# Optimization experiments

Hardware: AMD Instinct MI355X
Metric: run time of the kernel (lower is better)

Reference implementation:

```python
import jax, jax.numpy as jnp
import numpy as np

SORB = 64      # spin orbitals (sequence length)
NELE = 32      # electrons
H = 512        # num_hiddens
B = 4096       # batch
ALPHA = NELE // 2                      # = beta = 16 (spin-up / spin-down electrons)
MIN_I = min(SORB - 2 * ALPHA, 2 * ALPHA)  # = 32; symmetry mask active for i >= MIN_I
EPS = 1e-12


def setup_inputs() -> dict:
    key = jax.random.key(0)
    ks = jax.random.split(key, 10)
    s_in = 1.0 / np.sqrt(2.0)
    s_h = 1.0 / np.sqrt(H)
    return {
        "x": jax.random.randint(ks[0], (B, SORB), 0, 2, dtype=jnp.int32),  # occupancies {0,1}
        "W_ih0": jax.random.normal(ks[1], (3 * H, 2), jnp.float32) * s_in,   # GRU layer0 input weights (r,z,n)
        "W_hh0": jax.random.normal(ks[2], (3 * H, H), jnp.float32) * s_h,
        "W_ih1": jax.random.normal(ks[3], (3 * H, H), jnp.float32) * s_h,    # GRU layer1
        "W_hh1": jax.random.normal(ks[4], (3 * H, H), jnp.float32) * s_h,
        "W_amp": jax.random.normal(ks[5], (2, H), jnp.float32) * s_h,
        "b_amp": jax.random.normal(ks[6], (2,), jnp.float32) * 0.01,
        "W_phase": jax.random.normal(ks[7], (2, H), jnp.float32) * s_h,
        "b_phase": jax.random.normal(ks[8], (2,), jnp.float32) * 0.01,
    }


def _gru_cell(x_in, h, Wih, Whh):
    # PyTorch GRU (bias=False), gate order r, z, n
    gi = x_in @ Wih.T          # (B, 3H)
    gh = h @ Whh.T             # (B, 3H)
    r = jax.nn.sigmoid(gi[:, :H] + gh[:, :H])
    z = jax.nn.sigmoid(gi[:, H:2 * H] + gh[:, H:2 * H])
    n = jnp.tanh(gi[:, 2 * H:] + r * gh[:, 2 * H:])
    return (1.0 - z) * n + z * h


def reference(x, W_ih0, W_hh0, W_ih1, W_hh1, W_amp, b_amp, W_phase, b_phase):
    dt = W_ih0.dtype
    bits = x.astype(jnp.int32)           # (B, SORB) occupancies
    nb = bits.shape[0]

    def step(carry, inp):
        h0, h1, x0, amp, phase, nup, ndn = carry
        i, b_i = inp                      # site index, occupancy bits (B,)
        h0n = _gru_cell(x0, h0, W_ih0, W_hh0)
        h1n = _gru_cell(h0n, h1, W_ih1, W_hh1)
        y = h1n                           # (B, H)
        # amplitude: sqrt(softmax(linear))
        y_amp = jnp.sqrt(jax.nn.softmax(y @ W_amp.T + b_amp, axis=1))   # (B, 2)
        # phase: pi * softsign(linear)
        ph = y @ W_phase.T + b_phase
        y_ph = jnp.pi * ph / (1.0 + jnp.abs(ph))
        # particle-number symmetry mask (alpha == beta spin sectors)
        is_even = (i % 2) == 0            # even sites: spin-up, odd: spin-down
        cnt = jnp.where(is_even, nup, ndn)
        lower = (ALPHA - SORB // 2 + i // 2).astype(dt)
        occ_ok = (cnt < ALPHA).astype(dt)
        unocc_ok = (cnt > lower).astype(dt)
        mask = jnp.stack([unocc_ok, occ_ok], axis=1)
        masked = y_amp * mask
        masked = masked / jnp.sqrt(jnp.sum(masked * masked, axis=1, keepdims=True) + EPS)
        y_amp = jnp.where(i >= MIN_I, masked, y_amp)
        # accumulate conditional amplitude / phase at the sampled occupancy
        sel_a = jnp.take_along_axis(y_amp, b_i[:, None], axis=1)[:, 0]
        sel_p = jnp.take_along_axis(y_ph, b_i[:, None], axis=1)[:, 0]
        amp = amp * sel_a
        phase = phase + sel_p
        bf = b_i.astype(dt)
        nup = nup + jnp.where(is_even, bf, 0.0)
        ndn = ndn + jnp.where(is_even, 0.0, bf)
        x0n = jax.nn.one_hot(b_i, 2, dtype=dt)  # next-step GRU input
        return (h0n, h1n, x0n, amp, phase, nup, ndn), None

    init = (
        jnp.zeros((nb, H), dt), jnp.zeros((nb, H), dt), jnp.zeros((nb, 2), dt),
        jnp.ones((nb,), dt), jnp.zeros((nb,), dt), jnp.zeros((nb,), dt), jnp.zeros((nb,), dt),
    )
    xs = (jnp.arange(SORB), bits.T)       # scan over sites
    (_, _, _, amp, phase, _, _), _ = jax.lax.scan(step, init, xs)
    # complex wavefunction psi = amp * exp(1j*phase); returned as real pair (amp, phase)
    return jnp.stack([amp, phase], axis=-1)
```

## Files before the change

kernel.cpp:

```cpp
#include <hip/hip_runtime.h>
#include <hip/hip_bf16.h>

#define SORB  64
#define HID   512
#define BATCH 4096
#define N3H   1536
#define KD    512
#define BK    64
#define PI_F  3.14159265358979f

typedef _Float16 half8 __attribute__((ext_vector_type(8)));
typedef float    floatx4 __attribute__((ext_vector_type(4)));

__device__ __forceinline__ void gload16(const void* g, void* l) {
    __builtin_amdgcn_global_load_lds(
        (const __attribute__((address_space(1))) void*)g,
        (__attribute__((address_space(3))) void*)l, 16, 0, 0);
}

__device__ __forceinline__ float sigmoidf_(float x) { return 1.f / (1.f + __expf(-x)); }
__device__ __forceinline__ float tanhf_(float x) {
    x = fminf(fmaxf(x, -15.f), 15.f);
    const float e2 = __expf(2.f * x);
    return (e2 - 1.f) / (e2 + 1.f);
}

__global__ __launch_bounds__(256) void convw_kernel(
    const float* __restrict__ w0, const float* __restrict__ w1, const float* __restrict__ w2,
    _Float16* __restrict__ o0, _Float16* __restrict__ o1, _Float16* __restrict__ o2)
{
    const int i = blockIdx.x * 256 + threadIdx.x;
    if (i < N3H * KD) {
        o0[i] = (_Float16)w0[i];
        o1[i] = (_Float16)w1[i];
        o2[i] = (_Float16)w2[i];
    }
}

__global__ __launch_bounds__(256) void init_kernel(
    float* __restrict__ amp, float* __restrict__ phase,
    int* __restrict__ nup, int* __restrict__ ndn)
{
    const int i = blockIdx.x * 256 + threadIdx.x;
    if (i < BATCH) { amp[i] = 1.f; phase[i] = 0.f; nup[i] = 0; ndn[i] = 0; }
}


__global__ __launch_bounds__(256) void step1_kernel(
    const _Float16* __restrict__ h0h_c, const _Float16* __restrict__ h1h_c,
    const _Float16* __restrict__ wh0,   const _Float16* __restrict__ wh1,
    const float* __restrict__ Wih0, const int* __restrict__ bits,
    float* __restrict__ h0f, _Float16* __restrict__ h0h_n,
    _Float16* __restrict__ gB, int step)
{
    const int z = blockIdx.z;
    const _Float16* A = z ? h1h_c : h0h_c;
    const _Float16* W = z ? wh1 : wh0;
    const int j0 = blockIdx.x * 64;
    const int m0 = blockIdx.y * 64;

    __shared__ __align__(16) _Float16 As[64 * BK];
    __shared__ __align__(16) _Float16 Bs[192 * BK];

    const int tid  = threadIdx.x;
    const int lane = tid & 63;
    const int wid  = tid >> 6;
    const int wm   = wid >> 1, wj = wid & 1;

    floatx4 acc[2][2][3];
    const floatx4 z4 = {0.f, 0.f, 0.f, 0.f};
#pragma unroll
    for (int a = 0; a < 2; ++a)
#pragma unroll
        for (int b = 0; b < 2; ++b)
#pragma unroll
            for (int g = 0; g < 3; ++g) acc[a][b][g] = z4;

    const _Float16* a_srcp[2];
#pragma unroll
    for (int k2 = 0; k2 < 2; ++k2) {
        const int p = tid + k2 * 256, row = p >> 3, c = (p & 7) ^ (row & 7);
        a_srcp[k2] = A + (size_t)(m0 + row) * KD + c * 8;
    }
    const _Float16* b_srcp[6];
#pragma unroll
    for (int k2 = 0; k2 < 6; ++k2) {
        const int p = tid + k2 * 256, row = p >> 3, c = (p & 7) ^ (row & 7);
        const int grow = (row >> 6) * HID + j0 + (row & 63);
        b_srcp[k2] = W + (size_t)grow * KD + c * 8;
    }
    _Float16* a_dst[2];
#pragma unroll
    for (int k2 = 0; k2 < 2; ++k2) a_dst[k2] = As + (size_t)(k2 * 256 + wid * 64) * 8;
    _Float16* b_dst[6];
#pragma unroll
    for (int k2 = 0; k2 < 6; ++k2) b_dst[k2] = Bs + (size_t)(k2 * 256 + wid * 64) * 8;

    const int ku = lane >> 4;
    int aoff[2][2], boff[2][3][2];
#pragma unroll
    for (int mf = 0; mf < 2; ++mf) {
        const int r = wm * 32 + mf * 16 + (lane & 15);
#pragma unroll
        for (int kk = 0; kk < 2; ++kk)
            aoff[mf][kk] = r * BK + (((kk * 4 + ku) ^ (r & 7)) * 8);
    }
#pragma unroll
    for (int jf = 0; jf < 2; ++jf)
#pragma unroll
        for (int g = 0; g < 3; ++g) {
            const int r = g * 64 + wj * 32 + jf * 16 + (lane & 15);
#pragma unroll
            for (int kk = 0; kk < 2; ++kk)
                boff[jf][g][kk] = r * BK + (((kk * 4 + ku) ^ (r & 7)) * 8);
        }

    for (int kt = 0; kt < 8; ++kt) {
        const int k0 = kt * BK;
#pragma unroll
        for (int k2 = 0; k2 < 2; ++k2) gload16(a_srcp[k2] + k0, a_dst[k2]);
#pragma unroll
        for (int k2 = 0; k2 < 6; ++k2) gload16(b_srcp[k2] + k0, b_dst[k2]);
        __syncthreads();
#pragma unroll
        for (int kk = 0; kk < 2; ++kk) {
            half8 af[2], bf[2][3];
#pragma unroll
            for (int mf = 0; mf < 2; ++mf) af[mf] = *(const half8*)(As + aoff[mf][kk]);
#pragma unroll
            for (int jf = 0; jf < 2; ++jf)
#pragma unroll
                for (int g = 0; g < 3; ++g) bf[jf][g] = *(const half8*)(Bs + boff[jf][g][kk]);
#pragma unroll
            for (int mf = 0; mf < 2; ++mf)
#pragma unroll
                for (int jf = 0; jf < 2; ++jf)
#pragma unroll
                    for (int g = 0; g < 3; ++g)
                        acc[mf][jf][g] = __builtin_amdgcn_mfma_f32_16x16x32_f16(af[mf], bf[jf][g], acc[mf][jf][g], 0, 0, 0);
        }
        __syncthreads();
    }

    if (z == 0) {
#pragma unroll
        for (int mf = 0; mf < 2; ++mf)
#pragma unroll
            for (int jf = 0; jf < 2; ++jf) {
                const floatx4 gr = acc[mf][jf][0];
                const floatx4 gz = acc[mf][jf][1];
                const floatx4 gn = acc[mf][jf][2];
#pragma unroll
                for (int reg = 0; reg < 4; ++reg) {
                    const int m = m0 + wm * 32 + mf * 16 + (lane >> 4) * 4 + reg;
                    const int j = j0 + wj * 32 + jf * 16 + (lane & 15);
                    float gir = 0.f, giz = 0.f, gin = 0.f;
                    if (step > 0) {
                        const int t = bits[m * SORB + step - 1];
                        gir = Wih0[j * 2 + t];
                        giz = Wih0[(HID + j) * 2 + t];
                        gin = Wih0[(2 * HID + j) * 2 + t];
                    }
                    const float r  = sigmoidf_(gir + gr[reg]);
                    const float zz = sigmoidf_(giz + gz[reg]);
                    const float n  = tanhf_(gin + r * gn[reg]);
                    const size_t idx = (size_t)m * HID + j;
                    const float h  = h0f[idx];
                    const float hn = (1.f - zz) * n + zz * h;
                    h0f[idx]   = hn;
                    h0h_n[idx] = (_Float16)hn;
                }
            }
    } else {
#pragma unroll
        for (int mf = 0; mf < 2; ++mf)
#pragma unroll
            for (int jf = 0; jf < 2; ++jf)
#pragma unroll
                for (int g = 0; g < 3; ++g)
#pragma unroll
                    for (int reg = 0; reg < 4; ++reg) {
                        const int m = m0 + wm * 32 + mf * 16 + (lane >> 4) * 4 + reg;
                        const int j = j0 + wj * 32 + jf * 16 + (lane & 15);
                        gB[(size_t)m * N3H + g * HID + j] = (_Float16)acc[mf][jf][g][reg];
                    }
    }
}

__global__ __launch_bounds__(256) void step2_kernel(
    const _Float16* __restrict__ h0h_n, const _Float16* __restrict__ wi1,
    const _Float16* __restrict__ gB,
    float* __restrict__ h1f, _Float16* __restrict__ h1h_n)
{
    const int j0 = blockIdx.x * 64;
    const int m0 = blockIdx.y * 64;

    __shared__ __align__(16) _Float16 As[64 * BK];
    __shared__ __align__(16) _Float16 Bs[192 * BK];

    const int tid  = threadIdx.x;
    const int lane = tid & 63;
    const int wid  = tid >> 6;
    const int wm   = wid >> 1, wj = wid & 1;

    floatx4 acc[2][2][3];
    const floatx4 z4 = {0.f, 0.f, 0.f, 0.f};
#pragma unroll
    for (int a = 0; a < 2; ++a)
#pragma unroll
        for (int b = 0; b < 2; ++b)
#pragma unroll
            for (int g = 0; g < 3; ++g) acc[a][b][g] = z4;

    const _Float16* a_srcp[2];
#pragma unroll
    for (int k2 = 0; k2 < 2; ++k2) {
        const int p = tid + k2 * 256, row = p >> 3, c = (p & 7) ^ (row & 7);
        a_srcp[k2] = h0h_n + (size_t)(m0 + row) * KD + c * 8;
    }
    const _Float16* b_srcp[6];
#pragma unroll
    for (int k2 = 0; k2 < 6; ++k2) {
        const int p = tid + k2 * 256, row = p >> 3, c = (p & 7) ^ (row & 7);
        const int grow = (row >> 6) * HID + j0 + (row & 63);
        b_srcp[k2] = wi1 + (size_t)grow * KD + c * 8;
    }
    _Float16* a_dst[2];
#pragma unroll
    for (int k2 = 0; k2 < 2; ++k2) a_dst[k2] = As + (size_t)(k2 * 256 + wid * 64) * 8;
    _Float16* b_dst[6];
#pragma unroll
    for (int k2 = 0; k2 < 6; ++k2) b_dst[k2] = Bs + (size_t)(k2 * 256 + wid * 64) * 8;

    const int ku = lane >> 4;
    int aoff[2][2], boff[2][3][2];
#pragma unroll
    for (int mf = 0; mf < 2; ++mf) {
        const int r = wm * 32 + mf * 16 + (lane & 15);
#pragma unroll
        for (int kk = 0; kk < 2; ++kk)
            aoff[mf][kk] = r * BK + (((kk * 4 + ku) ^ (r & 7)) * 8);
    }
#pragma unroll
    for (int jf = 0; jf < 2; ++jf)
#pragma unroll
        for (int g = 0; g < 3; ++g) {
            const int r = g * 64 + wj * 32 + jf * 16 + (lane & 15);
#pragma unroll
            for (int kk = 0; kk < 2; ++kk)
                boff[jf][g][kk] = r * BK + (((kk * 4 + ku) ^ (r & 7)) * 8);
        }

    for (int kt = 0; kt < 8; ++kt) {
        const int k0 = kt * BK;
#pragma unroll
        for (int k2 = 0; k2 < 2; ++k2) gload16(a_srcp[k2] + k0, a_dst[k2]);
#pragma unroll
        for (int k2 = 0; k2 < 6; ++k2) gload16(b_srcp[k2] + k0, b_dst[k2]);
        __syncthreads();
#pragma unroll
        for (int kk = 0; kk < 2; ++kk) {
            half8 af[2], bf[2][3];
#pragma unroll
            for (int mf = 0; mf < 2; ++mf) af[mf] = *(const half8*)(As + aoff[mf][kk]);
#pragma unroll
            for (int jf = 0; jf < 2; ++jf)
#pragma unroll
                for (int g = 0; g < 3; ++g) bf[jf][g] = *(const half8*)(Bs + boff[jf][g][kk]);
#pragma unroll
            for (int mf = 0; mf < 2; ++mf)
#pragma unroll
                for (int jf = 0; jf < 2; ++jf)
#pragma unroll
                    for (int g = 0; g < 3; ++g)
                        acc[mf][jf][g] = __builtin_amdgcn_mfma_f32_16x16x32_f16(af[mf], bf[jf][g], acc[mf][jf][g], 0, 0, 0);
        }
        __syncthreads();
    }

#pragma unroll
    for (int mf = 0; mf < 2; ++mf)
#pragma unroll
        for (int jf = 0; jf < 2; ++jf) {
            const floatx4 gr = acc[mf][jf][0];
            const floatx4 gz = acc[mf][jf][1];
            const floatx4 gn = acc[mf][jf][2];
#pragma unroll
            for (int reg = 0; reg < 4; ++reg) {
                const int m = m0 + wm * 32 + mf * 16 + (lane >> 4) * 4 + reg;
                const int j = j0 + wj * 32 + jf * 16 + (lane & 15);
                const size_t gbase = (size_t)m * N3H;
                const float ghr = (float)gB[gbase + j];
                const float ghz = (float)gB[gbase + HID + j];
                const float ghn = (float)gB[gbase + 2 * HID + j];
                const float r  = sigmoidf_(gr[reg] + ghr);
                const float zz = sigmoidf_(gz[reg] + ghz);
                const float n  = tanhf_(gn[reg] + r * ghn);
                const size_t idx = (size_t)m * HID + j;
                const float h  = h1f[idx];
                const float hn = (1.f - zz) * n + zz * h;
                h1f[idx]   = hn;
                h1h_n[idx] = (_Float16)hn;
            }
        }
}

__global__ __launch_bounds__(256) void head_kernel(
    const _Float16* __restrict__ h1h_n,
    const float* __restrict__ Wamp, const float* __restrict__ bamp,
    const float* __restrict__ Wph,  const float* __restrict__ bph,
    const int* __restrict__ bits,
    float* __restrict__ amp, float* __restrict__ phase,
    int* __restrict__ nup, int* __restrict__ ndn,
    float* __restrict__ out, int step)
{
    const int lane = threadIdx.x & 63;
    const int m    = blockIdx.x * 4 + (threadIdx.x >> 6);
    const half8 hv = *(const half8*)(h1h_n + (size_t)m * HID + lane * 8);
    float d0 = 0.f, d1 = 0.f, d2 = 0.f, d3 = 0.f;
#pragma unroll
    for (int e = 0; e < 8; ++e) {
        const int j = lane * 8 + e;
        const float hn = (float)hv[e];
        d0 += hn * Wamp[j];       d1 += hn * Wamp[HID + j];
        d2 += hn * Wph[j];        d3 += hn * Wph[HID + j];
    }
#pragma unroll
    for (int off = 1; off < 64; off <<= 1) {
        d0 += __shfl_xor(d0, off); d1 += __shfl_xor(d1, off);
        d2 += __shfl_xor(d2, off); d3 += __shfl_xor(d3, off);
    }
    if (lane == 0) {
        const float a0 = d0 + bamp[0];
        const float a1 = d1 + bamp[1];
        const float mx = fmaxf(a0, a1);
        const float e0 = __expf(a0 - mx), e1 = __expf(a1 - mx);
        const float inv = 1.f / (e0 + e1);
        float ya0 = sqrtf(e0 * inv), ya1 = sqrtf(e1 * inv);
        const float p0 = d2 + bph[0];
        const float p1 = d3 + bph[1];
        const float yp0 = PI_F * p0 / (1.f + fabsf(p0));
        const float yp1 = PI_F * p1 / (1.f + fabsf(p1));
        const int even = ((step & 1) == 0);
        const int cnt = even ? nup[m] : ndn[m];
        if (step >= 32) {
            const int lower = (step >> 1) - 16;
            const float m0v = (cnt > lower) ? ya0 : 0.f;
            const float m1v = (cnt < 16) ? ya1 : 0.f;
            const float nrm = sqrtf(m0v * m0v + m1v * m1v + 1e-12f);
            ya0 = m0v / nrm; ya1 = m1v / nrm;
        }
        const int bi = bits[m * SORB + step];
        const float na = amp[m] * (bi ? ya1 : ya0);
        const float np = phase[m] + (bi ? yp1 : yp0);
        amp[m] = na; phase[m] = np;
        if (bi) { if (even) nup[m] = cnt + 1; else ndn[m] = cnt + 1; }
        if (step == SORB - 1) {
            out[m * 2 + 0] = na;
            out[m * 2 + 1] = np;
        }
    }
}

extern "C" void kernel_launch(void* const* d_in, const int* in_sizes, int n_in,
                              void* d_out, int out_size, void* d_ws, size_t ws_size,
                              hipStream_t stream) {
    const int*   bits = (const int*)d_in[0];
    const float* Wih0 = (const float*)d_in[1];
    const float* Whh0 = (const float*)d_in[2];
    const float* Wih1 = (const float*)d_in[3];
    const float* Whh1 = (const float*)d_in[4];
    const float* Wamp = (const float*)d_in[5];
    const float* bamp = (const float*)d_in[6];
    const float* Wph  = (const float*)d_in[7];
    const float* bph  = (const float*)d_in[8];
    float* out = (float*)d_out;

    char* ws = (char*)d_ws;
    size_t off = 0;
    auto alloc = [&](size_t bytes) {
        void* p = ws + off;
        off = (off + bytes + 255) & ~(size_t)255;
        return p;
    };
    _Float16* wh0 = (_Float16*)alloc((size_t)N3H * KD * 2);
    _Float16* wi1 = (_Float16*)alloc((size_t)N3H * KD * 2);
    _Float16* wh1 = (_Float16*)alloc((size_t)N3H * KD * 2);
    float*    h0f = (float*)alloc((size_t)BATCH * HID * 4);
    float*    h1f = (float*)alloc((size_t)BATCH * HID * 4);
    _Float16* h0hA = (_Float16*)alloc((size_t)BATCH * HID * 2);
    _Float16* h0hB = (_Float16*)alloc((size_t)BATCH * HID * 2);
    _Float16* h1hA = (_Float16*)alloc((size_t)BATCH * HID * 2);
    _Float16* h1hB = (_Float16*)alloc((size_t)BATCH * HID * 2);
    _Float16* gB  = (_Float16*)alloc((size_t)BATCH * N3H * 2);
    float*    amp   = (float*)alloc((size_t)BATCH * 4);
    float*    phase = (float*)alloc((size_t)BATCH * 4);
    int*      nup   = (int*)alloc((size_t)BATCH * 4);
    int*      ndn   = (int*)alloc((size_t)BATCH * 4);

    _Float16* h0h[2] = {h0hA, h0hB};
    _Float16* h1h[2] = {h1hA, h1hB};

    hipMemsetAsync(h0f, 0, (size_t)BATCH * HID * 4, stream);
    hipMemsetAsync(h1f, 0, (size_t)BATCH * HID * 4, stream);
    hipMemsetAsync(h0hA, 0, (size_t)BATCH * HID * 2, stream);
    hipMemsetAsync(h1hA, 0, (size_t)BATCH * HID * 2, stream);
    convw_kernel<<<(N3H * KD + 255) / 256, 256, 0, stream>>>(Whh0, Wih1, Whh1, wh0, wi1, wh1);
    init_kernel<<<BATCH / 256, 256, 0, stream>>>(amp, phase, nup, ndn);

    for (int s = 0; s < SORB; ++s) {
        const int cur = s & 1, nxt = cur ^ 1;
        step1_kernel<<<dim3(8, 64, 2), 256, 0, stream>>>(
            h0h[cur], h1h[cur], wh0, wh1, Wih0, bits, h0f, h0h[nxt], gB, s);
        step2_kernel<<<dim3(8, 64, 1), 256, 0, stream>>>(
            h0h[nxt], wi1, gB, h1f, h1h[nxt]);
        head_kernel<<<BATCH / 4, 256, 0, stream>>>(
            h1h[nxt], Wamp, bamp, Wph, bph, bits, amp, phase, nup, ndn, out, s);
    }
}
```

Baseline: 3.307 ms.

## Fuse per-step GRU kernels into one persistent cooperative kernel with grid syncs

Replaces the 192 separate launches (step1, step2, head per site) with a single persistent cooperative kernel that loops over the 64 sites and uses grid-wide syncs between phases. The head computation for step s-1 is folded into the start of step s, and the layer-1 GEMM is retiled to 32-row tiles to give more work items. This removes per-launch overhead and tail effects, at the cost of grid barrier latency and a block count limited by occupancy.

```diff
diff --git a/kernel.cpp b/kernel.cpp
--- a/kernel.cpp
+++ b/kernel.cpp
@@ -1,5 +1,8 @@
 #include <hip/hip_runtime.h>
 #include <hip/hip_bf16.h>
+#include <hip/hip_cooperative_groups.h>
+
+namespace cg = cooperative_groups;
 
 #define SORB  64
 #define HID   512
@@ -45,321 +48,309 @@
     if (i < BATCH) { amp[i] = 1.f; phase[i] = 0.f; nup[i] = 0; ndn[i] = 0; }
 }
 
-
-__global__ __launch_bounds__(256) void step1_kernel(
-    const _Float16* __restrict__ h0h_c, const _Float16* __restrict__ h1h_c,
-    const _Float16* __restrict__ wh0,   const _Float16* __restrict__ wh1,
-    const float* __restrict__ Wih0, const int* __restrict__ bits,
-    float* __restrict__ h0f, _Float16* __restrict__ h0h_n,
-    _Float16* __restrict__ gB, int step)
-{
-    const int z = blockIdx.z;
-    const _Float16* A = z ? h1h_c : h0h_c;
-    const _Float16* W = z ? wh1 : wh0;
-    const int j0 = blockIdx.x * 64;
-    const int m0 = blockIdx.y * 64;
-
-    __shared__ __align__(16) _Float16 As[64 * BK];
-    __shared__ __align__(16) _Float16 Bs[192 * BK];
-
-    const int tid  = threadIdx.x;
-    const int lane = tid & 63;
-    const int wid  = tid >> 6;
-    const int wm   = wid >> 1, wj = wid & 1;
-
-    floatx4 acc[2][2][3];
-    const floatx4 z4 = {0.f, 0.f, 0.f, 0.f};
-#pragma unroll
-    for (int a = 0; a < 2; ++a)
-#pragma unroll
-        for (int b = 0; b < 2; ++b)
-#pragma unroll
-            for (int g = 0; g < 3; ++g) acc[a][b][g] = z4;
-
-    const _Float16* a_srcp[2];
-#pragma unroll
-    for (int k2 = 0; k2 < 2; ++k2) {
-        const int p = tid + k2 * 256, row = p >> 3, c = (p & 7) ^ (row & 7);
-        a_srcp[k2] = A + (size_t)(m0 + row) * KD + c * 8;
-    }
-    const _Float16* b_srcp[6];
-#pragma unroll
-    for (int k2 = 0; k2 < 6; ++k2) {
-        const int p = tid + k2 * 256, row = p >> 3, c = (p & 7) ^ (row & 7);
-        const int grow = (row >> 6) * HID + j0 + (row & 63);
-        b_srcp[k2] = W + (size_t)grow * KD + c * 8;
-    }
-    _Float16* a_dst[2];
-#pragma unroll
-    for (int k2 = 0; k2 < 2; ++k2) a_dst[k2] = As + (size_t)(k2 * 256 + wid * 64) * 8;
-    _Float16* b_dst[6];
-#pragma unroll
-    for (int k2 = 0; k2 < 6; ++k2) b_dst[k2] = Bs + (size_t)(k2 * 256 + wid * 64) * 8;
-
-    const int ku = lane >> 4;
-    int aoff[2][2], boff[2][3][2];
-#pragma unroll
-    for (int mf = 0; mf < 2; ++mf) {
-        const int r = wm * 32 + mf * 16 + (lane & 15);
-#pragma unroll
-        for (int kk = 0; kk < 2; ++kk)
-            aoff[mf][kk] = r * BK + (((kk * 4 + ku) ^ (r & 7)) * 8);
-    }
-#pragma unroll
-    for (int jf = 0; jf < 2; ++jf)
-#pragma unroll
-        for (int g = 0; g < 3; ++g) {
-            const int r = g * 64 + wj * 32 + jf * 16 + (lane & 15);
-#pragma unroll
-            for (int kk = 0; kk < 2; ++kk)
-                boff[jf][g][kk] = r * BK + (((kk * 4 + ku) ^ (r & 7)) * 8);
-        }
-
-    for (int kt = 0; kt < 8; ++kt) {
-        const int k0 = kt * BK;
-#pragma unroll
-        for (int k2 = 0; k2 < 2; ++k2) gload16(a_srcp[k2] + k0, a_dst[k2]);
-#pragma unroll
-        for (int k2 = 0; k2 < 6; ++k2) gload16(b_srcp[k2] + k0, b_dst[k2]);
-        __syncthreads();
-#pragma unroll
-        for (int kk = 0; kk < 2; ++kk) {
-            half8 af[2], bf[2][3];
-#pragma unroll
-            for (int mf = 0; mf < 2; ++mf) af[mf] = *(const half8*)(As + aoff[mf][kk]);
-#pragma unroll
-            for (int jf = 0; jf < 2; ++jf)
-#pragma unroll
-                for (int g = 0; g < 3; ++g) bf[jf][g] = *(const half8*)(Bs + boff[jf][g][kk]);
-#pragma unroll
-            for (int mf = 0; mf < 2; ++mf)
-#pragma unroll
-                for (int jf = 0; jf < 2; ++jf)
-#pragma unroll
-                    for (int g = 0; g < 3; ++g)
-                        acc[mf][jf][g] = __builtin_amdgcn_mfma_f32_16x16x32_f16(af[mf], bf[jf][g], acc[mf][jf][g], 0, 0, 0);
-        }
-        __syncthreads();
-    }
-
-    if (z == 0) {
-#pragma unroll
-        for (int mf = 0; mf < 2; ++mf)
-#pragma unroll
-            for (int jf = 0; jf < 2; ++jf) {
-                const floatx4 gr = acc[mf][jf][0];
-                const floatx4 gz = acc[mf][jf][1];
-                const floatx4 gn = acc[mf][jf][2];
-#pragma unroll
-                for (int reg = 0; reg < 4; ++reg) {
-                    const int m = m0 + wm * 32 + mf * 16 + (lane >> 4) * 4 + reg;
-                    const int j = j0 + wj * 32 + jf * 16 + (lane & 15);
-                    float gir = 0.f, giz = 0.f, gin = 0.f;
-                    if (step > 0) {
-                        const int t = bits[m * SORB + step - 1];
-                        gir = Wih0[j * 2 + t];
-                        giz = Wih0[(HID + j) * 2 + t];
-                        gin = Wih0[(2 * HID + j) * 2 + t];
-                    }
-                    const float r  = sigmoidf_(gir + gr[reg]);
-                    const float zz = sigmoidf_(giz + gz[reg]);
-                    const float n  = tanhf_(gin + r * gn[reg]);
-                    const size_t idx = (size_t)m * HID + j;
-                    const float h  = h0f[idx];
-                    const float hn = (1.f - zz) * n + zz * h;
-                    h0f[idx]   = hn;
-                    h0h_n[idx] = (_Float16)hn;
-                }
-            }
-    } else {
-#pragma unroll
-        for (int mf = 0; mf < 2; ++mf)
-#pragma unroll
-            for (int jf = 0; jf < 2; ++jf)
-#pragma unroll
-                for (int g = 0; g < 3; ++g)
-#pragma unroll
-                    for (int reg = 0; reg < 4; ++reg) {
-                        const int m = m0 + wm * 32 + mf * 16 + (lane >> 4) * 4 + reg;
-                        const int j = j0 + wj * 32 + jf * 16 + (lane & 15);
-                        gB[(size_t)m * N3H + g * HID + j] = (_Float16)acc[mf][jf][g][reg];
-                    }
-    }
-}
-
-__global__ __launch_bounds__(256) void step2_kernel(
-    const _Float16* __restrict__ h0h_n, const _Float16* __restrict__ wi1,
-    const _Float16* __restrict__ gB,
-    float* __restrict__ h1f, _Float16* __restrict__ h1h_n)
-{
-    const int j0 = blockIdx.x * 64;
-    const int m0 = blockIdx.y * 64;
-
-    __shared__ __align__(16) _Float16 As[64 * BK];
-    __shared__ __align__(16) _Float16 Bs[192 * BK];
-
-    const int tid  = threadIdx.x;
-    const int lane = tid & 63;
-    const int wid  = tid >> 6;
-    const int wm   = wid >> 1, wj = wid & 1;
-
-    floatx4 acc[2][2][3];
-    const floatx4 z4 = {0.f, 0.f, 0.f, 0.f};
-#pragma unroll
-    for (int a = 0; a < 2; ++a)
-#pragma unroll
-        for (int b = 0; b < 2; ++b)
-#pragma unroll
-            for (int g = 0; g < 3; ++g) acc[a][b][g] = z4;
-
-    const _Float16* a_srcp[2];
-#pragma unroll
-    for (int k2 = 0; k2 < 2; ++k2) {
-        const int p = tid + k2 * 256, row = p >> 3, c = (p & 7) ^ (row & 7);
-        a_srcp[k2] = h0h_n + (size_t)(m0 + row) * KD + c * 8;
-    }
-    const _Float16* b_srcp[6];
-#pragma unroll
-    for (int k2 = 0; k2 < 6; ++k2) {
-        const int p = tid + k2 * 256, row = p >> 3, c = (p & 7) ^ (row & 7);
-        const int grow = (row >> 6) * HID + j0 + (row & 63);
-        b_srcp[k2] = wi1 + (size_t)grow * KD + c * 8;
-    }
-    _Float16* a_dst[2];
-#pragma unroll
-    for (int k2 = 0; k2 < 2; ++k2) a_dst[k2] = As + (size_t)(k2 * 256 + wid * 64) * 8;
-    _Float16* b_dst[6];
-#pragma unroll
-    for (int k2 = 0; k2 < 6; ++k2) b_dst[k2] = Bs + (size_t)(k2 * 256 + wid * 64) * 8;
-
-    const int ku = lane >> 4;
-    int aoff[2][2], boff[2][3][2];
-#pragma unroll
-    for (int mf = 0; mf < 2; ++mf) {
-        const int r = wm * 32 + mf * 16 + (lane & 15);
-#pragma unroll
-        for (int kk = 0; kk < 2; ++kk)
-            aoff[mf][kk] = r * BK + (((kk * 4 + ku) ^ (r & 7)) * 8);
-    }
-#pragma unroll
-    for (int jf = 0; jf < 2; ++jf)
-#pragma unroll
-        for (int g = 0; g < 3; ++g) {
-            const int r = g * 64 + wj * 32 + jf * 16 + (lane & 15);
-#pragma unroll
-            for (int kk = 0; kk < 2; ++kk)
-                boff[jf][g][kk] = r * BK + (((kk * 4 + ku) ^ (r & 7)) * 8);
-        }
-
-    for (int kt = 0; kt < 8; ++kt) {
-        const int k0 = kt * BK;
-#pragma unroll
-        for (int k2 = 0; k2 < 2; ++k2) gload16(a_srcp[k2] + k0, a_dst[k2]);
-#pragma unroll
-        for (int k2 = 0; k2 < 6; ++k2) gload16(b_srcp[k2] + k0, b_dst[k2]);
-        __syncthreads();
-#pragma unroll
-        for (int kk = 0; kk < 2; ++kk) {
-            half8 af[2], bf[2][3];
-#pragma unroll
-            for (int mf = 0; mf < 2; ++mf) af[mf] = *(const half8*)(As + aoff[mf][kk]);
-#pragma unroll
-            for (int jf = 0; jf < 2; ++jf)
-#pragma unroll
-                for (int g = 0; g < 3; ++g) bf[jf][g] = *(const half8*)(Bs + boff[jf][g][kk]);
-#pragma unroll
-            for (int mf = 0; mf < 2; ++mf)
-#pragma unroll
-                for (int jf = 0; jf < 2; ++jf)
-#pragma unroll
-                    for (int g = 0; g < 3; ++g)
-                        acc[mf][jf][g] = __builtin_amdgcn_mfma_f32_16x16x32_f16(af[mf], bf[jf][g], acc[mf][jf][g], 0, 0, 0);
-        }
-        __syncthreads();
-    }
-
-#pragma unroll
-    for (int mf = 0; mf < 2; ++mf)
-#pragma unroll
-        for (int jf = 0; jf < 2; ++jf) {
-            const floatx4 gr = acc[mf][jf][0];
-            const floatx4 gz = acc[mf][jf][1];
-            const floatx4 gn = acc[mf][jf][2];
-#pragma unroll
-            for (int reg = 0; reg < 4; ++reg) {
-                const int m = m0 + wm * 32 + mf * 16 + (lane >> 4) * 4 + reg;
-                const int j = j0 + wj * 32 + jf * 16 + (lane & 15);
-                const size_t gbase = (size_t)m * N3H;
-                const float ghr = (float)gB[gbase + j];
-                const float ghz = (float)gB[gbase + HID + j];
-                const float ghn = (float)gB[gbase + 2 * HID + j];
-                const float r  = sigmoidf_(gr[reg] + ghr);
-                const float zz = sigmoidf_(gz[reg] + ghz);
-                const float n  = tanhf_(gn[reg] + r * ghn);
-                const size_t idx = (size_t)m * HID + j;
-                const float h  = h1f[idx];
-                const float hn = (1.f - zz) * n + zz * h;
-                h1f[idx]   = hn;
-                h1h_n[idx] = (_Float16)hn;
-            }
-        }
-}
-
-__global__ __launch_bounds__(256) void head_kernel(
-    const _Float16* __restrict__ h1h_n,
+__device__ __forceinline__ void do_head(
+    const _Float16* __restrict__ h1, 
     const float* __restrict__ Wamp, const float* __restrict__ bamp,
     const float* __restrict__ Wph,  const float* __restrict__ bph,
     const int* __restrict__ bits,
     float* __restrict__ amp, float* __restrict__ phase,
     int* __restrict__ nup, int* __restrict__ ndn,
-    float* __restrict__ out, int step)
+    float* __restrict__ out, int step, int nb, int lane, int wid)
 {
-    const int lane = threadIdx.x & 63;
-    const int m    = blockIdx.x * 4 + (threadIdx.x >> 6);
-    const half8 hv = *(const half8*)(h1h_n + (size_t)m * HID + lane * 8);
-    float d0 = 0.f, d1 = 0.f, d2 = 0.f, d3 = 0.f;
-#pragma unroll
-    for (int e = 0; e < 8; ++e) {
-        const int j = lane * 8 + e;
-        const float hn = (float)hv[e];
-        d0 += hn * Wamp[j];       d1 += hn * Wamp[HID + j];
-        d2 += hn * Wph[j];        d3 += hn * Wph[HID + j];
+    for (int m = blockIdx.x * 4 + wid; m < BATCH; m += nb * 4) {
+        const half8 hv = *(const half8*)(h1 + (size_t)m * HID + lane * 8);
+        float d0 = 0.f, d1 = 0.f, d2 = 0.f, d3 = 0.f;
+#pragma unroll
+        for (int e = 0; e < 8; ++e) {
+            const int j = lane * 8 + e;
+            const float hn = (float)hv[e];
+            d0 += hn * Wamp[j];       d1 += hn * Wamp[HID + j];
+            d2 += hn * Wph[j];        d3 += hn * Wph[HID + j];
+        }
+#pragma unroll
+        for (int off = 1; off < 64; off <<= 1) {
+            d0 += __shfl_xor(d0, off); d1 += __shfl_xor(d1, off);
+            d2 += __shfl_xor(d2, off); d3 += __shfl_xor(d3, off);
+        }
+        if (lane == 0) {
+            const float a0 = d0 + bamp[0];
+            const float a1 = d1 + bamp[1];
+            const float mx = fmaxf(a0, a1);
+            const float e0 = __expf(a0 - mx), e1 = __expf(a1 - mx);
+            const float inv = 1.f / (e0 + e1);
+            float ya0 = sqrtf(e0 * inv), ya1 = sqrtf(e1 * inv);
+            const float p0 = d2 + bph[0];
+            const float p1 = d3 + bph[1];
+            const float yp0 = PI_F * p0 / (1.f + fabsf(p0));
+            const float yp1 = PI_F * p1 / (1.f + fabsf(p1));
+            const int even = ((step & 1) == 0);
+            const int cnt = even ? nup[m] : ndn[m];
+            if (step >= 32) {
+                const int lower = (step >> 1) - 16;
+                const float m0v = (cnt > lower) ? ya0 : 0.f;
+                const float m1v = (cnt < 16) ? ya1 : 0.f;
+                const float nrm = sqrtf(m0v * m0v + m1v * m1v + 1e-12f);
+                ya0 = m0v / nrm; ya1 = m1v / nrm;
+            }
+            const int bi = bits[m * SORB + step];
+            const float na = amp[m] * (bi ? ya1 : ya0);
+            const float np = phase[m] + (bi ? yp1 : yp0);
+            amp[m] = na; phase[m] = np;
+            if (bi) { if (even) nup[m] = cnt + 1; else ndn[m] = cnt + 1; }
+            if (step == SORB - 1) {
+                out[m * 2 + 0] = na;
+                out[m * 2 + 1] = np;
+            }
+        }
     }
-#pragma unroll
-    for (int off = 1; off < 64; off <<= 1) {
-        d0 += __shfl_xor(d0, off); d1 += __shfl_xor(d1, off);
-        d2 += __shfl_xor(d2, off); d3 += __shfl_xor(d3, off);
+}
+
+__global__ __launch_bounds__(256, 4) void fused_kernel(
+    _Float16* __restrict__ h0hA, _Float16* __restrict__ h0hB,
+    _Float16* __restrict__ h1hA, _Float16* __restrict__ h1hB,
+    const _Float16* __restrict__ wh0, const _Float16* __restrict__ wi1,
+    const _Float16* __restrict__ wh1,
+    const float* __restrict__ Wih0, const int* __restrict__ bits,
+    float* __restrict__ h0f, float* __restrict__ h1f, _Float16* __restrict__ gB,
+    const float* __restrict__ Wamp, const float* __restrict__ bamp,
+    const float* __restrict__ Wph,  const float* __restrict__ bph,
+    float* __restrict__ amp, float* __restrict__ phase,
+    int* __restrict__ nup, int* __restrict__ ndn, float* __restrict__ out)
+{
+    cg::grid_group gg = cg::this_grid();
+    __shared__ __align__(16) _Float16 smem[256 * BK];
+    _Float16* As = smem;
+    _Float16* Bs = smem + 64 * BK;
+
+    const int tid  = threadIdx.x;
+    const int lane = tid & 63;
+    const int wid  = tid >> 6;
+    const int wm   = wid >> 1, wj = wid & 1;
+    const int ku   = lane >> 4;
+    const int nb   = gridDim.x;
+
+    int aoff1[2][2];
+#pragma unroll
+    for (int mf = 0; mf < 2; ++mf) {
+        const int r = wm * 32 + mf * 16 + (lane & 15);
+#pragma unroll
+        for (int kk = 0; kk < 2; ++kk)
+            aoff1[mf][kk] = r * BK + (((kk * 4 + ku) ^ (r & 7)) * 8);
     }
-    if (lane == 0) {
-        const float a0 = d0 + bamp[0];
-        const float a1 = d1 + bamp[1];
-        const float mx = fmaxf(a0, a1);
-        const float e0 = __expf(a0 - mx), e1 = __expf(a1 - mx);
-        const float inv = 1.f / (e0 + e1);
-        float ya0 = sqrtf(e0 * inv), ya1 = sqrtf(e1 * inv);
-        const float p0 = d2 + bph[0];
-        const float p1 = d3 + bph[1];
-        const float yp0 = PI_F * p0 / (1.f + fabsf(p0));
-        const float yp1 = PI_F * p1 / (1.f + fabsf(p1));
-        const int even = ((step & 1) == 0);
-        const int cnt = even ? nup[m] : ndn[m];
-        if (step >= 32) {
-            const int lower = (step >> 1) - 16;
-            const float m0v = (cnt > lower) ? ya0 : 0.f;
-            const float m1v = (cnt < 16) ? ya1 : 0.f;
-            const float nrm = sqrtf(m0v * m0v + m1v * m1v + 1e-12f);
-            ya0 = m0v / nrm; ya1 = m1v / nrm;
-        }
-        const int bi = bits[m * SORB + step];
-        const float na = amp[m] * (bi ? ya1 : ya0);
-        const float np = phase[m] + (bi ? yp1 : yp0);
-        amp[m] = na; phase[m] = np;
-        if (bi) { if (even) nup[m] = cnt + 1; else ndn[m] = cnt + 1; }
-        if (step == SORB - 1) {
-            out[m * 2 + 0] = na;
-            out[m * 2 + 1] = np;
-        }
+    int aoff2[2];
+    {
+        const int r = wm * 16 + (lane & 15);
+#pragma unroll
+        for (int kk = 0; kk < 2; ++kk)
+            aoff2[kk] = r * BK + (((kk * 4 + ku) ^ (r & 7)) * 8);
     }
+    int boff[2][3][2];
+#pragma unroll
+    for (int jf = 0; jf < 2; ++jf)
+#pragma unroll
+        for (int g = 0; g < 3; ++g) {
+            const int r = g * 64 + wj * 32 + jf * 16 + (lane & 15);
+#pragma unroll
+            for (int kk = 0; kk < 2; ++kk)
+                boff[jf][g][kk] = r * BK + (((kk * 4 + ku) ^ (r & 7)) * 8);
+        }
+    _Float16* a_dst[2];
+#pragma unroll
+    for (int k2 = 0; k2 < 2; ++k2) a_dst[k2] = As + (size_t)(k2 * 256 + wid * 64) * 8;
+    _Float16* b_dst[6];
+#pragma unroll
+    for (int k2 = 0; k2 < 6; ++k2) b_dst[k2] = Bs + (size_t)(k2 * 256 + wid * 64) * 8;
+
+#pragma unroll 1
+    for (int s = 0; s < SORB; ++s) {
+        _Float16* h0c = (s & 1) ? h0hB : h0hA;
+        _Float16* h0n = (s & 1) ? h0hA : h0hB;
+        _Float16* h1c = (s & 1) ? h1hB : h1hA;
+        _Float16* h1n = (s & 1) ? h1hA : h1hB;
+
+        if (s > 0)
+            do_head(h1c, Wamp, bamp, Wph, bph, bits, amp, phase, nup, ndn,
+                    out, s - 1, nb, lane, wid);
+
+        for (int t = blockIdx.x; t < 1024; t += nb) {
+            const int z  = t >> 9;
+            const int j0 = (t & 7) * 64;
+            const int m0 = ((t >> 3) & 63) * 64;
+            const _Float16* Aop = z ? h1c : h0c;
+            const _Float16* Wop = z ? wh1 : wh0;
+
+            floatx4 acc[2][2][3];
+            const floatx4 z4 = {0.f, 0.f, 0.f, 0.f};
+#pragma unroll
+            for (int a = 0; a < 2; ++a)
+#pragma unroll
+                for (int b = 0; b < 2; ++b)
+#pragma unroll
+                    for (int g = 0; g < 3; ++g) acc[a][b][g] = z4;
+
+            const _Float16* a_srcp[2];
+#pragma unroll
+            for (int k2 = 0; k2 < 2; ++k2) {
+                const int p = tid + k2 * 256, row = p >> 3, c = (p & 7) ^ (row & 7);
+                a_srcp[k2] = Aop + (size_t)(m0 + row) * KD + c * 8;
+            }
+            const _Float16* b_srcp[6];
+#pragma unroll
+            for (int k2 = 0; k2 < 6; ++k2) {
+                const int p = tid + k2 * 256, row = p >> 3, c = (p & 7) ^ (row & 7);
+                const int grow = (row >> 6) * HID + j0 + (row & 63);
+                b_srcp[k2] = Wop + (size_t)grow * KD + c * 8;
+            }
+
+            for (int kt = 0; kt < 8; ++kt) {
+                const int k0 = kt * BK;
+#pragma unroll
+                for (int k2 = 0; k2 < 2; ++k2) gload16(a_srcp[k2] + k0, a_dst[k2]);
+#pragma unroll
+                for (int k2 = 0; k2 < 6; ++k2) gload16(b_srcp[k2] + k0, b_dst[k2]);
+                __syncthreads();
+#pragma unroll
+                for (int kk = 0; kk < 2; ++kk) {
+                    half8 af[2], bf[2][3];
+#pragma unroll
+                    for (int mf = 0; mf < 2; ++mf) af[mf] = *(const half8*)(As + aoff1[mf][kk]);
+#pragma unroll
+                    for (int jf = 0; jf < 2; ++jf)
+#pragma unroll
+                        for (int g = 0; g < 3; ++g) bf[jf][g] = *(const half8*)(Bs + boff[jf][g][kk]);
+#pragma unroll
+                    for (int mf = 0; mf < 2; ++mf)
+#pragma unroll
+                        for (int jf = 0; jf < 2; ++jf)
+#pragma unroll
+                            for (int g = 0; g < 3; ++g)
+                                acc[mf][jf][g] = __builtin_amdgcn_mfma_f32_16x16x32_f16(
+                                    af[mf], bf[jf][g], acc[mf][jf][g], 0, 0, 0);
+                }
+                __syncthreads();
+            }
+
+            if (z == 0) {
+#pragma unroll
+                for (int mf = 0; mf < 2; ++mf)
+#pragma unroll
+                    for (int jf = 0; jf < 2; ++jf) {
+                        const floatx4 gr = acc[mf][jf][0];
+                        const floatx4 gz = acc[mf][jf][1];
+                        const floatx4 gn = acc[mf][jf][2];
+#pragma unroll
+                        for (int reg = 0; reg < 4; ++reg) {
+                            const int m = m0 + wm * 32 + mf * 16 + (lane >> 4) * 4 + reg;
+                            const int j = j0 + wj * 32 + jf * 16 + (lane & 15);
+                            float gir = 0.f, giz = 0.f, gin = 0.f;
+                            if (s > 0) {
+                                const int tb = bits[m * SORB + s - 1];
+                                gir = Wih0[j * 2 + tb];
+                                giz = Wih0[(HID + j) * 2 + tb];
+                                gin = Wih0[(2 * HID + j) * 2 + tb];
+                            }
+                            const float r  = sigmoidf_(gir + gr[reg]);
+                            const float zz = sigmoidf_(giz + gz[reg]);
+                            const float n  = tanhf_(gin + r * gn[reg]);
+                            const size_t idx = (size_t)m * HID + j;
+                            const float h  = h0f[idx];
+                            const float hn = (1.f - zz) * n + zz * h;
+                            h0f[idx] = hn;
+                            h0n[idx] = (_Float16)hn;
+                        }
+                    }
+            } else {
+#pragma unroll
+                for (int mf = 0; mf < 2; ++mf)
+#pragma unroll
+                    for (int jf = 0; jf < 2; ++jf)
+#pragma unroll
+                        for (int g = 0; g < 3; ++g)
+#pragma unroll
+                            for (int reg = 0; reg < 4; ++reg) {
+                                const int m = m0 + wm * 32 + mf * 16 + (lane >> 4) * 4 + reg;
+                                const int j = j0 + wj * 32 + jf * 16 + (lane & 15);
+                                gB[(size_t)m * N3H + g * HID + j] = (_Float16)acc[mf][jf][g][reg];
+                            }
+            }
+        }
+        gg.sync();
+
+        for (int t = blockIdx.x; t < 1024; t += nb) {
+            const int j0 = (t & 7) * 64;
+            const int m0 = (t >> 3) * 32;
+
+            floatx4 acc2[2][3];
+            const floatx4 z4 = {0.f, 0.f, 0.f, 0.f};
+#pragma unroll
+            for (int b = 0; b < 2; ++b)
+#pragma unroll
+                for (int g = 0; g < 3; ++g) acc2[b][g] = z4;
+
+            const int p = tid, rowA = p >> 3, cA = (p & 7) ^ (rowA & 7);
+            const _Float16* a_src = h0n + (size_t)(m0 + rowA) * KD + cA * 8;
+            const _Float16* b_srcp[6];
+#pragma unroll
+            for (int k2 = 0; k2 < 6; ++k2) {
+                const int q = tid + k2 * 256, row = q >> 3, c = (q & 7) ^ (row & 7);
+                const int grow = (row >> 6) * HID + j0 + (row & 63);
+                b_srcp[k2] = wi1 + (size_t)grow * KD + c * 8;
+            }
+
+            for (int kt = 0; kt < 8; ++kt) {
+                const int k0 = kt * BK;
+                gload16(a_src + k0, a_dst[0]);
+#pragma unroll
+                for (int k2 = 0; k2 < 6; ++k2) gload16(b_srcp[k2] + k0, b_dst[k2]);
+                __syncthreads();
+#pragma unroll
+                for (int kk = 0; kk < 2; ++kk) {
+                    half8 af;
+                    af = *(const half8*)(As + aoff2[kk]);
+                    half8 bf[2][3];
+#pragma unroll
+                    for (int jf = 0; jf < 2; ++jf)
+#pragma unroll
+                        for (int g = 0; g < 3; ++g) bf[jf][g] = *(const half8*)(Bs + boff[jf][g][kk]);
+#pragma unroll
+                    for (int jf = 0; jf < 2; ++jf)
+#pragma unroll
+                        for (int g = 0; g < 3; ++g)
+                            acc2[jf][g] = __builtin_amdgcn_mfma_f32_16x16x32_f16(
+                                af, bf[jf][g], acc2[jf][g], 0, 0, 0);
+                }
+                __syncthreads();
+            }
+
+#pragma unroll
+            for (int jf = 0; jf < 2; ++jf) {
+                const floatx4 gr = acc2[jf][0];
+                const floatx4 gz = acc2[jf][1];
+                const floatx4 gn = acc2[jf][2];
+#pragma unroll
+                for (int reg = 0; reg < 4; ++reg) {
+                    const int m = m0 + wm * 16 + (lane >> 4) * 4 + reg;
+                    const int j = j0 + wj * 32 + jf * 16 + (lane & 15);
+                    const size_t gbase = (size_t)m * N3H;
+                    const float ghr = (float)gB[gbase + j];
+                    const float ghz = (float)gB[gbase + HID + j];
+                    const float ghn = (float)gB[gbase + 2 * HID + j];
+                    const float r  = sigmoidf_(gr[reg] + ghr);
+                    const float zz = sigmoidf_(gz[reg] + ghz);
+                    const float n  = tanhf_(gn[reg] + r * ghn);
+                    const size_t idx = (size_t)m * HID + j;
+                    const float h  = h1f[idx];
+                    const float hn = (1.f - zz) * n + zz * h;
+                    h1f[idx] = hn;
+                    h1n[idx] = (_Float16)hn;
+                }
+            }
+        }
+        gg.sync();
+    }
+
+    do_head(h1hA, Wamp, bamp, Wph, bph, bits, amp, phase, nup, ndn,
+            out, SORB - 1, nb, lane, wid);
 }
 
 extern "C" void kernel_launch(void* const* d_in, const int* in_sizes, int n_in,
@@ -398,9 +389,6 @@
     int*      nup   = (int*)alloc((size_t)BATCH * 4);
     int*      ndn   = (int*)alloc((size_t)BATCH * 4);
 
-    _Float16* h0h[2] = {h0hA, h0hB};
-    _Float16* h1h[2] = {h1hA, h1hB};
-
     hipMemsetAsync(h0f, 0, (size_t)BATCH * HID * 4, stream);
     hipMemsetAsync(h1f, 0, (size_t)BATCH * HID * 4, stream);
     hipMemsetAsync(h0hA, 0, (size_t)BATCH * HID * 2, stream);
@@ -408,13 +396,19 @@
     convw_kernel<<<(N3H * KD + 255) / 256, 256, 0, stream>>>(Whh0, Wih1, Whh1, wh0, wi1, wh1);
     init_kernel<<<BATCH / 256, 256, 0, stream>>>(amp, phase, nup, ndn);
 
-    for (int s = 0; s < SORB; ++s) {
-        const int cur = s & 1, nxt = cur ^ 1;
-        step1_kernel<<<dim3(8, 64, 2), 256, 0, stream>>>(
-            h0h[cur], h1h[cur], wh0, wh1, Wih0, bits, h0f, h0h[nxt], gB, s);
-        step2_kernel<<<dim3(8, 64, 1), 256, 0, stream>>>(
-            h0h[nxt], wi1, gB, h1f, h1h[nxt]);
-        head_kernel<<<BATCH / 4, 256, 0, stream>>>(
-            h1h[nxt], Wamp, bamp, Wph, bph, bits, amp, phase, nup, ndn, out, s);
-    }
-}
+    int maxb = 0;
+    hipOccupancyMaxActiveBlocksPerMultiprocessor(&maxb, fused_kernel, 256, 0);
+    int nblocks = maxb * 256;
+    if (nblocks > 1024) nblocks = 1024;
+    if (nblocks < 256)  nblocks = 256;
+
+    void* kargs[] = {
+        (void*)&h0hA, (void*)&h0hB, (void*)&h1hA, (void*)&h1hB,
+        (void*)&wh0, (void*)&wi1, (void*)&wh1,
+        (void*)&Wih0, (void*)&bits,
+        (void*)&h0f, (void*)&h1f, (void*)&gB,
+        (void*)&Wamp, (void*)&bamp, (void*)&Wph, (void*)&bph,
+        (void*)&amp, (void*)&phase, (void*)&nup, (void*)&ndn, (void*)&out
+    };
+    hipLaunchCooperativeKernel(fused_kernel, dim3(nblocks), dim3(256), kargs, 0, stream);
+}
```

Result: slower. 12.39 ms (+274.7%).
